# Kernel tuning notes

Measured on AMD Instinct MI355X. Metric: run time of the kernel, lower is better.

Reference implementation:

```python
import jax, jax.numpy as jnp
import numpy as np

N_HEADS = 16

def setup_inputs() -> dict:
    key = jax.random.key(0)
    k1, k2 = jax.random.split(key)
    B, S, H = 4, 2048, 1024
    hidden_states = jax.random.normal(k1, (B, S, H), dtype=jnp.float32)
    # F.linear weight: [out_features, in_features]; init std per module
    std = 0.02 / np.sqrt(2.0 * 24 * H)
    queries_weight = jax.random.normal(k2, (H, H), dtype=jnp.float32) * std
    return {"hidden_states": hidden_states, "queries_weight": queries_weight}


def reference(hidden_states, queries_weight):
    B, S, H = hidden_states.shape
    hd = H // N_HEADS
    # F.linear: x @ W^T
    q = hidden_states @ queries_weight.T
    qh = q.reshape(B, S, N_HEADS, hd)          # [B,S,h,d]
    xh = hidden_states.reshape(B, S, N_HEADS, hd)
    # pre_attn = Q K^T (no softmax), then attn @ V with K=V=x heads
    pre_attn = jnp.einsum('bqhd,bkhd->bhqk', qh, xh)   # [B,h,S,S]
    attn = jnp.einsum('bhqk,bkhd->bqhd', pre_attn, xh) # [B,S,h,d]
    return attn.reshape(B, S, H)
```

## Files before the change

### kernel.cpp

```cpp
#include <hip/hip_runtime.h>
#include <hip/hip_bf16.h>


typedef __bf16 bf16x8 __attribute__((ext_vector_type(8)));
typedef float f32x4 __attribute__((ext_vector_type(4)));

typedef __attribute__((address_space(3))) unsigned int lds_u32;
typedef const __attribute__((address_space(1))) unsigned int glb_u32;

__device__ __forceinline__ void gld_lds16(const void* g, void* l) {
    __builtin_amdgcn_global_load_lds((glb_u32*)g, (lds_u32*)l, 16, 0, 0);
}

__device__ __forceinline__ unsigned short f2bf(float f) {
    unsigned int u = __float_as_uint(f);
    u += 0x7FFFu + ((u >> 16) & 1u);
    return (unsigned short)(u >> 16);
}

__global__ __launch_bounds__(256) void convert_kernel(
        const float* __restrict__ x, const float* __restrict__ W,
        unsigned short* __restrict__ xb, unsigned short* __restrict__ Wb) {
    int t = blockIdx.x * 256 + threadIdx.x;
    const float* src; unsigned short* dst; size_t idx;
    if (t < 2097152) { src = x; dst = xb; idx = (size_t)t * 4; }
    else             { src = W; dst = Wb; idx = (size_t)(t - 2097152) * 4; }
    float4 v = *(const float4*)&src[idx];
    ushort4 o;
    o.x = f2bf(v.x); o.y = f2bf(v.y); o.z = f2bf(v.z); o.w = f2bf(v.w);
    *(ushort4*)&dst[idx] = o;
}

__global__ __launch_bounds__(256) void g_partial(
        const float* __restrict__ x, float* __restrict__ Gp) {
    __shared__ __align__(16) float xr[32 * 64];
    const int tid = threadIdx.x;
    const int chunk = blockIdx.x;
    const int bh = blockIdx.y;
    const int b = bh >> 4, h = bh & 15;
    const int d0  = (tid >> 4) * 4;
    const int dp0 = (tid & 15) * 4;
    const float* xbase = x + ((size_t)(b * 2048 + chunk * 128)) * 1024 + h * 64;
    float acc[4][4] = {};
    for (int p = 0; p < 4; ++p) {
        __syncthreads();
        #pragma unroll
        for (int i = 0; i < 2; ++i) {
            int l = tid + 256 * i;
            int r = l >> 4;
            int c = (l & 15) * 4;
            *(float4*)&xr[r * 64 + c] =
                *(const float4*)&xbase[(size_t)(p * 32 + r) * 1024 + c];
        }
        __syncthreads();
        #pragma unroll 8
        for (int r = 0; r < 32; ++r) {
            float4 a = *(const float4*)&xr[r * 64 + d0];
            float4 v = *(const float4*)&xr[r * 64 + dp0];
            float av[4] = {a.x, a.y, a.z, a.w};
            float vv[4] = {v.x, v.y, v.z, v.w};
            #pragma unroll
            for (int u = 0; u < 4; ++u)
                #pragma unroll
                for (int w = 0; w < 4; ++w)
                    acc[u][w] += av[u] * vv[w];
        }
    }
    float* gp = Gp + ((size_t)(chunk * 64 + bh)) * 4096;
    #pragma unroll
    for (int u = 0; u < 4; ++u)
        #pragma unroll
        for (int w = 0; w < 4; ++w)
            gp[(d0 + u) * 64 + dp0 + w] = acc[u][w];
}

__global__ __launch_bounds__(256) void g_reduce(
        const float* __restrict__ Gp, unsigned short* __restrict__ Gb) {
    const int bh = blockIdx.x;
    const int e0 = blockIdx.y * 1024 + threadIdx.x * 4;
    float4 s = {0.f, 0.f, 0.f, 0.f};
    #pragma unroll
    for (int c = 0; c < 16; ++c) {
        float4 v = *(const float4*)&Gp[((size_t)(c * 64 + bh)) * 4096 + e0];
        s.x += v.x; s.y += v.y; s.z += v.z; s.w += v.w;
    }
    ushort4 o;
    o.x = f2bf(s.x); o.y = f2bf(s.y); o.z = f2bf(s.z); o.w = f2bf(s.w);
    *(ushort4*)&Gb[(size_t)bh * 4096 + e0] = o;
}

__global__ __launch_bounds__(256) void gemm_q(
        const unsigned short* __restrict__ X, const unsigned short* __restrict__ Wb,
        unsigned short* __restrict__ Q) {
    __shared__ __align__(16) unsigned short lA[128 * 64];
    __shared__ __align__(16) unsigned short lB[128 * 64];
    const int tid = threadIdx.x;
    const int m0 = blockIdx.y * 128;
    const int n0 = blockIdx.x * 128;
    const int lane = tid & 63;
    const int wave = tid >> 6;
    const int wr = (wave >> 1) * 64;
    const int wc = (wave & 1) * 64;
    const int lm = lane & 15;
    const int quad = lane >> 4;

    const int srow = wave * 32 + (lane >> 3);
    const int scol = (lane & 7) * 8;

    f32x4 acc[4][4] = {};

    for (int kt = 0; kt < 1024; kt += 64) {
        const unsigned short* ga = &X [(size_t)(m0 + srow) * 1024 + kt + scol];
        const unsigned short* gb = &Wb[(size_t)(n0 + srow) * 1024 + kt + scol];
        #pragma unroll
        for (int i = 0; i < 4; ++i) {
            gld_lds16(ga + (size_t)i * 8 * 1024, &lA[(wave * 32 + i * 8) * 64]);
            gld_lds16(gb + (size_t)i * 8 * 1024, &lB[(wave * 32 + i * 8) * 64]);
        }
        __syncthreads();
        #pragma unroll
        for (int kk = 0; kk < 2; ++kk) {
            bf16x8 af[4], bg[4];
            #pragma unroll
            for (int mi = 0; mi < 4; ++mi)
                af[mi] = *(const bf16x8*)&lA[(wr + mi * 16 + lm) * 64 + kk * 32 + quad * 8];
            #pragma unroll
            for (int ni = 0; ni < 4; ++ni)
                bg[ni] = *(const bf16x8*)&lB[(wc + ni * 16 + lm) * 64 + kk * 32 + quad * 8];
            #pragma unroll
            for (int mi = 0; mi < 4; ++mi)
                #pragma unroll
                for (int ni = 0; ni < 4; ++ni)
                    acc[mi][ni] = __builtin_amdgcn_mfma_f32_16x16x32_bf16(
                        af[mi], bg[ni], acc[mi][ni], 0, 0, 0);
        }
        __syncthreads();
    }
    #pragma unroll
    for (int mi = 0; mi < 4; ++mi)
        #pragma unroll
        for (int ni = 0; ni < 4; ++ni)
            #pragma unroll
            for (int r = 0; r < 4; ++r) {
                int row = m0 + wr + mi * 16 + quad * 4 + r;
                int col = n0 + wc + ni * 16 + lm;
                Q[(size_t)row * 1024 + col] = f2bf(acc[mi][ni][r]);
            }
}

#define LDK 72
__global__ __launch_bounds__(256) void gemm_out(
        const unsigned short* __restrict__ Q, const unsigned short* __restrict__ Gb,
        float* __restrict__ out) {
    __shared__ __align__(16) unsigned short lA[128 * LDK];
    __shared__ __align__(16) unsigned short lB[64 * LDK];
    const int tid = threadIdx.x;
    const int h  = blockIdx.x;
    const int s0 = blockIdx.y * 128;
    const int b  = s0 >> 11;
    const int bh = b * 16 + h;
    const int lane = tid & 63;
    const int wave = tid >> 6;
    const int lm = lane & 15;
    const int quad = lane >> 4;

    #pragma unroll
    for (int i = 0; i < 4; ++i) {
        int l = tid + 256 * i;
        int r = l >> 3;
        int c = (l & 7) * 8;
        *(uint4*)&lA[r * LDK + c] = *(const uint4*)&Q[(size_t)(s0 + r) * 1024 + h * 64 + c];
    }
    #pragma unroll
    for (int i = 0; i < 2; ++i) {
        int l = tid + 256 * i;
        int r = l >> 3;
        int c = (l & 7) * 8;
        *(uint4*)&lB[r * LDK + c] = *(const uint4*)&Gb[(size_t)bh * 4096 + r * 64 + c];
    }
    __syncthreads();
    f32x4 acc[2][4] = {};
    #pragma unroll
    for (int kk = 0; kk < 2; ++kk) {
        bf16x8 af[2], bg[4];
        #pragma unroll
        for (int mi = 0; mi < 2; ++mi)
            af[mi] = *(const bf16x8*)&lA[(wave * 32 + mi * 16 + lm) * LDK + kk * 32 + quad * 8];
        #pragma unroll
        for (int ni = 0; ni < 4; ++ni)
            bg[ni] = *(const bf16x8*)&lB[(ni * 16 + lm) * LDK + kk * 32 + quad * 8];
        #pragma unroll
        for (int mi = 0; mi < 2; ++mi)
            #pragma unroll
            for (int ni = 0; ni < 4; ++ni)
                acc[mi][ni] = __builtin_amdgcn_mfma_f32_16x16x32_bf16(
                    af[mi], bg[ni], acc[mi][ni], 0, 0, 0);
    }
    #pragma unroll
    for (int mi = 0; mi < 2; ++mi)
        #pragma unroll
        for (int ni = 0; ni < 4; ++ni)
            #pragma unroll
            for (int r = 0; r < 4; ++r) {
                int row = s0 + wave * 32 + mi * 16 + quad * 4 + r;
                int col = h * 64 + ni * 16 + lm;
                out[(size_t)row * 1024 + col] = acc[mi][ni][r];
            }
}

extern "C" void kernel_launch(void* const* d_in, const int* in_sizes, int n_in,
                              void* d_out, int out_size, void* d_ws, size_t ws_size,
                              hipStream_t stream) {
    const float* x = (const float*)d_in[0];
    const float* W = (const float*)d_in[1];
    float* out = (float*)d_out;
    char* ws = (char*)d_ws;
    unsigned short* xb = (unsigned short*)(ws);
    unsigned short* Wb = (unsigned short*)(ws + 16777216);
    unsigned short* Qb = (unsigned short*)(ws + 18874368);
    float*          Gp = (float*)        (ws + 35651584);
    unsigned short* Gb = (unsigned short*)(ws + 52428864);

    convert_kernel<<<9216, 256, 0, stream>>>(x, W, xb, Wb);
    g_partial<<<dim3(16, 64), 256, 0, stream>>>(x, Gp);
    g_reduce<<<dim3(64, 4), 256, 0, stream>>>(Gp, Gb);
    gemm_q<<<dim3(8, 64), 256, 0, stream>>>(xb, Wb, Qb);
    gemm_out<<<dim3(16, 64), 256, 0, stream>>>(Qb, Gb, out);
}
```

Measured before the change: 140.8 us.

## Fuse x conversion into Gram kernel, use MFMA, and fuse Q GEMM with output GEMM

Folds the bf16 conversion of x into the per-head Gram partial kernel, which now stages a transposed bf16 tile in LDS and computes x^T x with MFMA instead of scalar FP32 FMAs. The Q projection GEMM and the per-head Q·G GEMM are fused, so the Q tile stays in LDS and is never written to or reread from global memory. This removes one kernel launch and the Q round trip, but the Gram products now accumulate from bf16 inputs rather than fp32, which lowers precision. The fused kernel also uses more LDS per block, which may reduce occupancy.

```diff
diff --git a/kernel.cpp b/kernel.cpp
--- a/kernel.cpp
+++ b/kernel.cpp
@@ -18,60 +18,58 @@
     return (unsigned short)(u >> 16);
 }
 
-__global__ __launch_bounds__(256) void convert_kernel(
-        const float* __restrict__ x, const float* __restrict__ W,
-        unsigned short* __restrict__ xb, unsigned short* __restrict__ Wb) {
+__global__ __launch_bounds__(256) void convert_w(
+        const float* __restrict__ W, unsigned short* __restrict__ Wb) {
     int t = blockIdx.x * 256 + threadIdx.x;
-    const float* src; unsigned short* dst; size_t idx;
-    if (t < 2097152) { src = x; dst = xb; idx = (size_t)t * 4; }
-    else             { src = W; dst = Wb; idx = (size_t)(t - 2097152) * 4; }
-    float4 v = *(const float4*)&src[idx];
+    float4 v = *(const float4*)&W[(size_t)t * 4];
     ushort4 o;
     o.x = f2bf(v.x); o.y = f2bf(v.y); o.z = f2bf(v.z); o.w = f2bf(v.w);
-    *(ushort4*)&dst[idx] = o;
-}
-
-__global__ __launch_bounds__(256) void g_partial(
-        const float* __restrict__ x, float* __restrict__ Gp) {
-    __shared__ __align__(16) float xr[32 * 64];
+    *(ushort4*)&Wb[(size_t)t * 4] = o;
+}
+
+#define XT_S 136
+__global__ __launch_bounds__(256) void gx_partial(
+        const float* __restrict__ x, unsigned short* __restrict__ xb,
+        float* __restrict__ Gp) {
+    __shared__ __align__(16) unsigned short xt[64 * XT_S];
     const int tid = threadIdx.x;
     const int chunk = blockIdx.x;
     const int bh = blockIdx.y;
     const int b = bh >> 4, h = bh & 15;
-    const int d0  = (tid >> 4) * 4;
-    const int dp0 = (tid & 15) * 4;
-    const float* xbase = x + ((size_t)(b * 2048 + chunk * 128)) * 1024 + h * 64;
-    float acc[4][4] = {};
-    for (int p = 0; p < 4; ++p) {
-        __syncthreads();
-        #pragma unroll
-        for (int i = 0; i < 2; ++i) {
-            int l = tid + 256 * i;
-            int r = l >> 4;
-            int c = (l & 15) * 4;
-            *(float4*)&xr[r * 64 + c] =
-                *(const float4*)&xbase[(size_t)(p * 32 + r) * 1024 + c];
+    const size_t gbase = ((size_t)(b * 2048 + chunk * 128)) * 1024 + h * 64;
+    #pragma unroll
+    for (int i = 0; i < 8; ++i) {
+        int idx = tid + 256 * i;
+        int s = idx >> 4;
+        int c = (idx & 15) * 4;
+        float4 v = *(const float4*)&x[gbase + (size_t)s * 1024 + c];
+        ushort4 o;
+        o.x = f2bf(v.x); o.y = f2bf(v.y); o.z = f2bf(v.z); o.w = f2bf(v.w);
+        *(ushort4*)&xb[gbase + (size_t)s * 1024 + c] = o;
+        xt[(c + 0) * XT_S + s] = o.x;
+        xt[(c + 1) * XT_S + s] = o.y;
+        xt[(c + 2) * XT_S + s] = o.z;
+        xt[(c + 3) * XT_S + s] = o.w;
+    }
+    __syncthreads();
+    const int wave = tid >> 6, lane = tid & 63;
+    const int lm = lane & 15, quad = lane >> 4;
+    f32x4 acc[4] = {};
+    #pragma unroll
+    for (int k = 0; k < 4; ++k) {
+        bf16x8 af = *(const bf16x8*)&xt[(wave * 16 + lm) * XT_S + k * 32 + quad * 8];
+        #pragma unroll
+        for (int ni = 0; ni < 4; ++ni) {
+            bf16x8 bg = *(const bf16x8*)&xt[(ni * 16 + lm) * XT_S + k * 32 + quad * 8];
+            acc[ni] = __builtin_amdgcn_mfma_f32_16x16x32_bf16(af, bg, acc[ni], 0, 0, 0);
         }
-        __syncthreads();
-        #pragma unroll 8
-        for (int r = 0; r < 32; ++r) {
-            float4 a = *(const float4*)&xr[r * 64 + d0];
-            float4 v = *(const float4*)&xr[r * 64 + dp0];
-            float av[4] = {a.x, a.y, a.z, a.w};
-            float vv[4] = {v.x, v.y, v.z, v.w};
-            #pragma unroll
-            for (int u = 0; u < 4; ++u)
-                #pragma unroll
-                for (int w = 0; w < 4; ++w)
-                    acc[u][w] += av[u] * vv[w];
-        }
     }
     float* gp = Gp + ((size_t)(chunk * 64 + bh)) * 4096;
     #pragma unroll
-    for (int u = 0; u < 4; ++u)
-        #pragma unroll
-        for (int w = 0; w < 4; ++w)
-            gp[(d0 + u) * 64 + dp0 + w] = acc[u][w];
+    for (int ni = 0; ni < 4; ++ni)
+        #pragma unroll
+        for (int r = 0; r < 4; ++r)
+            gp[(wave * 16 + quad * 4 + r) * 64 + ni * 16 + lm] = acc[ni][r];
 }
 
 __global__ __launch_bounds__(256) void g_reduce(
@@ -89,28 +87,38 @@
     *(ushort4*)&Gb[(size_t)bh * 4096 + e0] = o;
 }
 
-__global__ __launch_bounds__(256) void gemm_q(
-        const unsigned short* __restrict__ X, const unsigned short* __restrict__ Wb,
-        unsigned short* __restrict__ Q) {
-    __shared__ __align__(16) unsigned short lA[128 * 64];
-    __shared__ __align__(16) unsigned short lB[128 * 64];
+__global__ __launch_bounds__(256) void gemm_qout(
+        const unsigned short* __restrict__ xb, const unsigned short* __restrict__ Wb,
+        const unsigned short* __restrict__ Gb, float* __restrict__ out) {
+    __shared__ __align__(16) unsigned short smem[26624];
+    unsigned short* lA = smem;
+    unsigned short* lB = smem + 8192;
+    unsigned short* Qt = smem;
+    unsigned short* G2 = smem + 17408;
     const int tid = threadIdx.x;
+    const int n0 = blockIdx.x * 128;
     const int m0 = blockIdx.y * 128;
-    const int n0 = blockIdx.x * 128;
-    const int lane = tid & 63;
-    const int wave = tid >> 6;
-    const int wr = (wave >> 1) * 64;
-    const int wc = (wave & 1) * 64;
-    const int lm = lane & 15;
-    const int quad = lane >> 4;
-
+    const int b  = blockIdx.y >> 4;
+    const int h0 = blockIdx.x * 2;
+    const int lane = tid & 63, wave = tid >> 6;
+    const int wr = (wave >> 1) * 64, wc = (wave & 1) * 64;
+    const int lm = lane & 15, quad = lane >> 4;
     const int srow = wave * 32 + (lane >> 3);
     const int scol = (lane & 7) * 8;
 
+    #pragma unroll
+    for (int i = 0; i < 4; ++i) {
+        int idx = tid + 256 * i;
+        int hh = idx >> 9;
+        int rr = (idx >> 3) & 63;
+        int cc = (idx & 7) * 8;
+        *(uint4*)&G2[hh * 4608 + rr * 72 + cc] =
+            *(const uint4*)&Gb[((size_t)(b * 16 + h0 + hh)) * 4096 + rr * 64 + cc];
+    }
+
     f32x4 acc[4][4] = {};
-
     for (int kt = 0; kt < 1024; kt += 64) {
-        const unsigned short* ga = &X [(size_t)(m0 + srow) * 1024 + kt + scol];
+        const unsigned short* ga = &xb[(size_t)(m0 + srow) * 1024 + kt + scol];
         const unsigned short* gb = &Wb[(size_t)(n0 + srow) * 1024 + kt + scol];
         #pragma unroll
         for (int i = 0; i < 4; ++i) {
@@ -141,71 +149,39 @@
         #pragma unroll
         for (int ni = 0; ni < 4; ++ni)
             #pragma unroll
-            for (int r = 0; r < 4; ++r) {
-                int row = m0 + wr + mi * 16 + quad * 4 + r;
-                int col = n0 + wc + ni * 16 + lm;
-                Q[(size_t)row * 1024 + col] = f2bf(acc[mi][ni][r]);
-            }
-}
-
-#define LDK 72
-__global__ __launch_bounds__(256) void gemm_out(
-        const unsigned short* __restrict__ Q, const unsigned short* __restrict__ Gb,
-        float* __restrict__ out) {
-    __shared__ __align__(16) unsigned short lA[128 * LDK];
-    __shared__ __align__(16) unsigned short lB[64 * LDK];
-    const int tid = threadIdx.x;
-    const int h  = blockIdx.x;
-    const int s0 = blockIdx.y * 128;
-    const int b  = s0 >> 11;
-    const int bh = b * 16 + h;
-    const int lane = tid & 63;
-    const int wave = tid >> 6;
-    const int lm = lane & 15;
-    const int quad = lane >> 4;
-
-    #pragma unroll
-    for (int i = 0; i < 4; ++i) {
-        int l = tid + 256 * i;
-        int r = l >> 3;
-        int c = (l & 7) * 8;
-        *(uint4*)&lA[r * LDK + c] = *(const uint4*)&Q[(size_t)(s0 + r) * 1024 + h * 64 + c];
-    }
-    #pragma unroll
-    for (int i = 0; i < 2; ++i) {
-        int l = tid + 256 * i;
-        int r = l >> 3;
-        int c = (l & 7) * 8;
-        *(uint4*)&lB[r * LDK + c] = *(const uint4*)&Gb[(size_t)bh * 4096 + r * 64 + c];
-    }
-    __syncthreads();
-    f32x4 acc[2][4] = {};
+            for (int r = 0; r < 4; ++r)
+                Qt[(wr + mi * 16 + quad * 4 + r) * 136 + wc + ni * 16 + lm] =
+                    f2bf(acc[mi][ni][r]);
+    #pragma unroll
+    for (int mi = 0; mi < 4; ++mi)
+        #pragma unroll
+        for (int ni = 0; ni < 4; ++ni)
+            acc[mi][ni] = (f32x4){0.f, 0.f, 0.f, 0.f};
+    const int hh = wave & 1;
     #pragma unroll
     for (int kk = 0; kk < 2; ++kk) {
-        bf16x8 af[2], bg[4];
-        #pragma unroll
-        for (int mi = 0; mi < 2; ++mi)
-            af[mi] = *(const bf16x8*)&lA[(wave * 32 + mi * 16 + lm) * LDK + kk * 32 + quad * 8];
-        #pragma unroll
-        for (int ni = 0; ni < 4; ++ni)
-            bg[ni] = *(const bf16x8*)&lB[(ni * 16 + lm) * LDK + kk * 32 + quad * 8];
-        #pragma unroll
-        for (int mi = 0; mi < 2; ++mi)
+        bf16x8 af[4], bg[4];
+        #pragma unroll
+        for (int mi = 0; mi < 4; ++mi)
+            af[mi] = *(const bf16x8*)&Qt[(wr + mi * 16 + lm) * 136 + wc + kk * 32 + quad * 8];
+        #pragma unroll
+        for (int ni = 0; ni < 4; ++ni)
+            bg[ni] = *(const bf16x8*)&G2[hh * 4608 + (ni * 16 + lm) * 72 + kk * 32 + quad * 8];
+        #pragma unroll
+        for (int mi = 0; mi < 4; ++mi)
             #pragma unroll
             for (int ni = 0; ni < 4; ++ni)
                 acc[mi][ni] = __builtin_amdgcn_mfma_f32_16x16x32_bf16(
                     af[mi], bg[ni], acc[mi][ni], 0, 0, 0);
     }
     #pragma unroll
-    for (int mi = 0; mi < 2; ++mi)
-        #pragma unroll
-        for (int ni = 0; ni < 4; ++ni)
-            #pragma unroll
-            for (int r = 0; r < 4; ++r) {
-                int row = s0 + wave * 32 + mi * 16 + quad * 4 + r;
-                int col = h * 64 + ni * 16 + lm;
-                out[(size_t)row * 1024 + col] = acc[mi][ni][r];
-            }
+    for (int mi = 0; mi < 4; ++mi)
+        #pragma unroll
+        for (int ni = 0; ni < 4; ++ni)
+            #pragma unroll
+            for (int r = 0; r < 4; ++r)
+                out[(size_t)(m0 + wr + mi * 16 + quad * 4 + r) * 1024
+                    + n0 + wc + ni * 16 + lm] = acc[mi][ni][r];
 }
 
 extern "C" void kernel_launch(void* const* d_in, const int* in_sizes, int n_in,
@@ -217,13 +193,11 @@
     char* ws = (char*)d_ws;
     unsigned short* xb = (unsigned short*)(ws);
     unsigned short* Wb = (unsigned short*)(ws + 16777216);
-    unsigned short* Qb = (unsigned short*)(ws + 18874368);
-    float*          Gp = (float*)        (ws + 35651584);
-    unsigned short* Gb = (unsigned short*)(ws + 52428864);
-
-    convert_kernel<<<9216, 256, 0, stream>>>(x, W, xb, Wb);
-    g_partial<<<dim3(16, 64), 256, 0, stream>>>(x, Gp);
+    float*          Gp = (float*)        (ws + 18874368);
+    unsigned short* Gb = (unsigned short*)(ws + 35651584);
+
+    convert_w<<<1024, 256, 0, stream>>>(W, Wb);
+    gx_partial<<<dim3(16, 64), 256, 0, stream>>>(x, xb, Gp);
     g_reduce<<<dim3(64, 4), 256, 0, stream>>>(Gp, Gb);
-    gemm_q<<<dim3(8, 64), 256, 0, stream>>>(xb, Wb, Qb);
-    gemm_out<<<dim3(16, 64), 256, 0, stream>>>(Qb, Gb, out);
-}
+    gemm_qout<<<dim3(8, 64), 256, 0, stream>>>(xb, Wb, Gb, out);
+}
```

Measured after the change: 125.2 us. 11.1% less time.
